# Kernel optimization log

Measured on AMD Instinct MI355X. Metric: run time of the kernel, lower is better.

The kernel has to match this reference:

```python
import jax, jax.numpy as jnp
import numpy as np

B = 32768      # rows
L = 512        # sequence_length
H = 1024       # inter_layer_size
E = 128        # encoding_size
K = 8          # number of (shifting_type, transformer_ID) combinations / decoders


def setup_inputs() -> dict:
    key = jax.random.key(0)
    ks = jax.random.split(key, 8)
    feats = jax.random.normal(ks[0], (B, L), jnp.float32)
    ids = jax.random.randint(ks[1], (B,), 0, K).astype(jnp.float32)
    x = jnp.concatenate([feats, ids[:, None]], axis=1)  # [B, L+1], last col = combination ID

    def init_w(k, shape, fan_in):
        return jax.random.normal(k, shape, jnp.float32) / np.float32(np.sqrt(fan_in))

    # shared encoder: Linear(L->H), Linear(H->E)  (weights stored [in, out])
    We1 = init_w(ks[2], (L, H), L); be1 = jnp.zeros((H,), jnp.float32)
    We2 = init_w(ks[3], (H, E), H); be2 = jnp.zeros((E,), jnp.float32)
    # per-ID decoders stacked along expert dim K: Linear(E->H), Linear(H->L)
    Wd1 = init_w(ks[4], (K, E, H), E); bd1 = jnp.zeros((K, H), jnp.float32)
    Wd2 = init_w(ks[5], (K, H, L), H); bd2 = jnp.zeros((K, L), jnp.float32)
    return dict(x=x, We1=We1, be1=be1, We2=We2, be2=be2,
                Wd1=Wd1, bd1=bd1, Wd2=Wd2, bd2=bd2)


def reference(x, We1, be1, We2, be2, Wd1, bd1, Wd2, bd2):
    seq_len = We1.shape[0]
    n_experts = Wd1.shape[0]
    ids = x[:, seq_len].astype(jnp.int32)          # routing column
    # torch code emits rows grouped by unique ID (torch.unique returns sorted ids);
    # jnp.argsort is stable, so within-group original order is preserved.
    order = jnp.argsort(ids)
    xs = x[order, :seq_len]                        # [B, L] grouped features
    ids_s = ids[order]                             # [B]

    # shared encoder MLP (LeakyReLU slope 0.01, torch default)
    h = jax.nn.leaky_relu(xs @ We1 + be1)          # [B, H]
    z = jax.nn.leaky_relu(h @ We2 + be2)           # [B, E]

    # dense expert dispatch: run every decoder, select per-row expert via one-hot
    hd = jax.nn.leaky_relu(jnp.einsum('be,keh->kbh', z, Wd1) + bd1[:, None, :])  # [K, B, H]
    y_all = jnp.einsum('kbh,khl->kbl', hd, Wd2) + bd2[:, None, :]                # [K, B, L]
    onehot = (ids_s[None, :] == jnp.arange(n_experts)[:, None]).astype(y_all.dtype)  # [K, B]
    return jnp.einsum('kb,kbl->bl', onehot, y_all)  # [B, L]
```

## Files before the change

### kernel.cpp

```cpp
#include <hip/hip_runtime.h>
#include <hip/hip_bf16.h>

#define B_ROWS 32768
#define L_DIM 512
#define H_DIM 1024
#define E_DIM 128
#define K_EXP 8
#define NBLK 128

typedef __bf16 bf16x8 __attribute__((ext_vector_type(8)));
typedef float f32x4 __attribute__((ext_vector_type(4)));

__device__ __forceinline__ void gload16(const void* src, void* dst) {
    __builtin_amdgcn_global_load_lds(
        (const __attribute__((address_space(1))) unsigned int*)src,
        (__attribute__((address_space(3))) unsigned int*)dst, 16, 0, 0);
}

__global__ void k_ids_hist(const float* __restrict__ x, int* __restrict__ ids,
                           int* __restrict__ hist) {
    __shared__ int lh[K_EXP];
    int t = threadIdx.x;
    if (t < K_EXP) lh[t] = 0;
    __syncthreads();
    int i = blockIdx.x * 256 + t;
    int id = (int)x[(size_t)i * (L_DIM + 1) + L_DIM];
    ids[i] = id;
    atomicAdd(&lh[id], 1);
    __syncthreads();
    if (t < K_EXP) hist[blockIdx.x * K_EXP + t] = lh[t];
}

__global__ void k_scan(const int* __restrict__ hist, int* __restrict__ base,
                       int* __restrict__ seg, int* __restrict__ tp) {
    __shared__ int c[K_EXP];
    __shared__ int sseg[K_EXP + 1];
    int k = threadIdx.x;
    if (k < K_EXP) {
        int run = 0;
        for (int b = 0; b < NBLK; ++b) {
            base[b * K_EXP + k] = run;
            run += hist[b * K_EXP + k];
        }
        c[k] = run;
    }
    __syncthreads();
    if (k == 0) {
        int s = 0, t2 = 0;
        for (int e = 0; e < K_EXP; ++e) {
            sseg[e] = s; seg[e] = s; tp[e] = t2;
            s += c[e]; t2 += (c[e] + 127) >> 7;
        }
        sseg[K_EXP] = s; seg[K_EXP] = s; tp[K_EXP] = t2;
    }
    __syncthreads();
    if (k < K_EXP) {
        int s0 = sseg[k];
        for (int b = 0; b < NBLK; ++b) base[b * K_EXP + k] += s0;
    }
}

__global__ void k_order(const int* __restrict__ ids, const int* __restrict__ base,
                        int* __restrict__ order) {
    __shared__ int sid[256];
    int t = threadIdx.x;
    int i = blockIdx.x * 256 + t;
    int my = ids[i];
    sid[t] = my;
    __syncthreads();
    int rank = 0;
    for (int j = 0; j < t; ++j) rank += (sid[j] == my) ? 1 : 0;
    order[base[blockIdx.x * K_EXP + my] + rank] = i;
}

__global__ void k_gather(const float* __restrict__ x, const int* __restrict__ order,
                         __hip_bfloat16* __restrict__ xs) {
    int idx = blockIdx.x * 256 + threadIdx.x;
    int p = idx >> 7;
    int c4 = (idx & 127) << 2;
    int src = order[p];
    const float* sp = x + (size_t)src * (L_DIM + 1) + c4;
    __hip_bfloat16 v[4];
    v[0] = __float2bfloat16(sp[0]);
    v[1] = __float2bfloat16(sp[1]);
    v[2] = __float2bfloat16(sp[2]);
    v[3] = __float2bfloat16(sp[3]);
    *(uint2*)(xs + (size_t)p * L_DIM + c4) = *(uint2*)v;
}

__global__ void k_transpose(const float* __restrict__ W, __hip_bfloat16* __restrict__ Wt,
                            int KDim, int NDim) {
    __shared__ float tile[32][33];
    int k0 = blockIdx.x << 5, n0 = blockIdx.y << 5;
    const float* Wb = W + (size_t)blockIdx.z * KDim * NDim;
    __hip_bfloat16* Wtb = Wt + (size_t)blockIdx.z * KDim * NDim;
    int tx = threadIdx.x & 31, ty = threadIdx.x >> 5;
    for (int i = ty; i < 32; i += 8)
        tile[i][tx] = Wb[(size_t)(k0 + i) * NDim + n0 + tx];
    __syncthreads();
    for (int i = ty; i < 32; i += 8)
        Wtb[(size_t)(n0 + i) * KDim + k0 + tx] = __float2bfloat16(tile[tx][i]);
}

template <int KD, int ND, bool GROUPED, bool LEAKY, bool OUT_BF16>
__launch_bounds__(256)
__global__ void gemm_mfma(const __hip_bfloat16* __restrict__ A,
                          const __hip_bfloat16* __restrict__ Bt,
                          const float* __restrict__ bias,
                          void* __restrict__ Cout,
                          const int* __restrict__ seg, const int* __restrict__ tp) {
    __shared__ __align__(16) __hip_bfloat16 smem[2 * 2 * 128 * 32];
    const int t = threadIdx.x;
    const int w = t >> 6, l = t & 63;
    const int n0 = blockIdx.y << 7;
    int m0, mEnd;
    const __hip_bfloat16* Bp = Bt;
    const float* bp = bias;
    if (GROUPED) {
        int bx = blockIdx.x;
        if (bx >= tp[K_EXP]) return;
        int e = 0;
        while (bx >= tp[e + 1]) ++e;
        m0 = seg[e] + ((bx - tp[e]) << 7);
        mEnd = seg[e + 1];
        Bp += (size_t)e * KD * ND;
        bp += (size_t)e * ND;
    } else {
        m0 = blockIdx.x << 7;
        mEnd = m0 + 128;
    }
    const int wm = w >> 1, wn = w & 1;
    const int g = l >> 4, li = l & 15;

    f32x4 acc[4][4];
#pragma unroll
    for (int i = 0; i < 4; ++i)
#pragma unroll
        for (int j = 0; j < 4; ++j) acc[i][j] = (f32x4){0.f, 0.f, 0.f, 0.f};

    auto stage = [&](int buf, int kt) {
#pragma unroll
        for (int qi = 0; qi < 2; ++qi) {
            int q = 2 * w + qi;
            int r = q * 16 + (l >> 2);
            int s = l & 3;
            int ksg = s ^ ((r >> 1) & 3);
            int rowg = m0 + r;
            if (GROUPED) rowg = min(rowg, B_ROWS - 1);
            const __hip_bfloat16* src = A + (size_t)rowg * KD + kt * 32 + ksg * 8;
            gload16(src, &smem[(buf * 2 + 0) * 4096 + q * 512]);
        }
#pragma unroll
        for (int qi = 0; qi < 2; ++qi) {
            int q = 2 * w + qi;
            int rc = q * 16 + (l >> 2);
            int s = l & 3;
            int ksg = s ^ ((rc >> 1) & 3);
            const __hip_bfloat16* src = Bp + (size_t)(n0 + rc) * KD + kt * 32 + ksg * 8;
            gload16(src, &smem[(buf * 2 + 1) * 4096 + q * 512]);
        }
    };

    constexpr int NK = KD / 32;
    stage(0, 0);
    for (int kt = 0; kt < NK; ++kt) {
        int buf = kt & 1;
        __syncthreads();
        if (kt + 1 < NK) stage(buf ^ 1, kt + 1);
        bf16x8 af[4], bfr[4];
#pragma unroll
        for (int fm = 0; fm < 4; ++fm) {
            int rr = wm * 64 + fm * 16 + li;
            int ss = g ^ ((rr >> 1) & 3);
            af[fm] = *(const bf16x8*)&smem[(buf * 2 + 0) * 4096 + rr * 32 + ss * 8];
        }
#pragma unroll
        for (int fn = 0; fn < 4; ++fn) {
            int cc = wn * 64 + fn * 16 + li;
            int ss = g ^ ((cc >> 1) & 3);
            bfr[fn] = *(const bf16x8*)&smem[(buf * 2 + 1) * 4096 + cc * 32 + ss * 8];
        }
#pragma unroll
        for (int fm = 0; fm < 4; ++fm)
#pragma unroll
            for (int fn = 0; fn < 4; ++fn)
                acc[fm][fn] = __builtin_amdgcn_mfma_f32_16x16x32_bf16(
                    af[fm], bfr[fn], acc[fm][fn], 0, 0, 0);
    }

    float bv[4];
#pragma unroll
    for (int fn = 0; fn < 4; ++fn) bv[fn] = bp[n0 + wn * 64 + fn * 16 + li];
#pragma unroll
    for (int fm = 0; fm < 4; ++fm) {
#pragma unroll
        for (int i = 0; i < 4; ++i) {
            int r = m0 + wm * 64 + fm * 16 + g * 4 + i;
            if (!GROUPED || r < mEnd) {
#pragma unroll
                for (int fn = 0; fn < 4; ++fn) {
                    float v = acc[fm][fn][i] + bv[fn];
                    if (LEAKY) v = v > 0.f ? v : 0.01f * v;
                    size_t off = (size_t)r * ND + n0 + wn * 64 + fn * 16 + li;
                    if (OUT_BF16)
                        ((__hip_bfloat16*)Cout)[off] = __float2bfloat16(v);
                    else
                        ((float*)Cout)[off] = v;
                }
            }
        }
    }
}

extern "C" void kernel_launch(void* const* d_in, const int* in_sizes, int n_in,
                              void* d_out, int out_size, void* d_ws, size_t ws_size,
                              hipStream_t stream) {
    (void)in_sizes; (void)n_in; (void)out_size; (void)ws_size;
    const float* x   = (const float*)d_in[0];
    const float* We1 = (const float*)d_in[1];
    const float* be1 = (const float*)d_in[2];
    const float* We2 = (const float*)d_in[3];
    const float* be2 = (const float*)d_in[4];
    const float* Wd1 = (const float*)d_in[5];
    const float* bd1 = (const float*)d_in[6];
    const float* Wd2 = (const float*)d_in[7];
    const float* bd2 = (const float*)d_in[8];
    float* out = (float*)d_out;

    char* w = (char*)d_ws;
    auto alloc = [&](size_t bytes) {
        char* p = w;
        w += (bytes + 255) & ~(size_t)255;
        return p;
    };
    int* ids   = (int*)alloc((size_t)B_ROWS * 4);
    int* order = (int*)alloc((size_t)B_ROWS * 4);
    int* hist  = (int*)alloc((size_t)NBLK * K_EXP * 4);
    int* base  = (int*)alloc((size_t)NBLK * K_EXP * 4);
    int* seg   = (int*)alloc((K_EXP + 1) * 4);
    int* tp    = (int*)alloc((K_EXP + 1) * 4);
    __hip_bfloat16* xs   = (__hip_bfloat16*)alloc((size_t)B_ROWS * L_DIM * 2);
    __hip_bfloat16* hbuf = (__hip_bfloat16*)alloc((size_t)B_ROWS * H_DIM * 2);
    __hip_bfloat16* zbuf = (__hip_bfloat16*)alloc((size_t)B_ROWS * E_DIM * 2);
    __hip_bfloat16* Wt1  = (__hip_bfloat16*)alloc((size_t)L_DIM * H_DIM * 2);
    __hip_bfloat16* Wt2  = (__hip_bfloat16*)alloc((size_t)H_DIM * E_DIM * 2);
    __hip_bfloat16* Wd1t = (__hip_bfloat16*)alloc((size_t)K_EXP * E_DIM * H_DIM * 2);
    __hip_bfloat16* Wd2t = (__hip_bfloat16*)alloc((size_t)K_EXP * H_DIM * L_DIM * 2);

    k_ids_hist<<<NBLK, 256, 0, stream>>>(x, ids, hist);
    k_scan<<<1, 64, 0, stream>>>(hist, base, seg, tp);
    k_order<<<NBLK, 256, 0, stream>>>(ids, base, order);
    k_gather<<<(B_ROWS * (L_DIM / 4)) / 256, 256, 0, stream>>>(x, order, xs);

    k_transpose<<<dim3(L_DIM / 32, H_DIM / 32, 1), 256, 0, stream>>>(We1, Wt1, L_DIM, H_DIM);
    k_transpose<<<dim3(H_DIM / 32, E_DIM / 32, 1), 256, 0, stream>>>(We2, Wt2, H_DIM, E_DIM);
    k_transpose<<<dim3(E_DIM / 32, H_DIM / 32, K_EXP), 256, 0, stream>>>(Wd1, Wd1t, E_DIM, H_DIM);
    k_transpose<<<dim3(H_DIM / 32, L_DIM / 32, K_EXP), 256, 0, stream>>>(Wd2, Wd2t, H_DIM, L_DIM);

    gemm_mfma<L_DIM, H_DIM, false, true, true>
        <<<dim3(B_ROWS / 128, H_DIM / 128), 256, 0, stream>>>(xs, Wt1, be1, hbuf, nullptr, nullptr);
    gemm_mfma<H_DIM, E_DIM, false, true, true>
        <<<dim3(B_ROWS / 128, E_DIM / 128), 256, 0, stream>>>(hbuf, Wt2, be2, zbuf, nullptr, nullptr);
    gemm_mfma<E_DIM, H_DIM, true, true, true>
        <<<dim3(B_ROWS / 128 + K_EXP, H_DIM / 128), 256, 0, stream>>>(zbuf, Wd1t, bd1, hbuf, seg, tp);
    gemm_mfma<H_DIM, L_DIM, true, false, false>
        <<<dim3(B_ROWS / 128 + K_EXP, L_DIM / 128), 256, 0, stream>>>(hbuf, Wd2t, bd2, out, seg, tp);
}
```

Baseline: 224.8 us.

## Fuse encoder GEMMs with LDS-resident hidden tile and pad expert segments

Fuses the two encoder GEMMs into one kernel. Each 128-row block computes 128-column chunks of the hidden layer, keeps them in LDS as bf16 and feeds them straight into the second GEMM, so the hidden activation never goes to global memory. Expert segments are padded to 128-row multiples with a per-tile expert map, which removes the per-block expert search and row clamping. Decoder output rows are remapped to compact positions at store time, and decoder blocks are swizzled across the grid. The trade-off is low occupancy in the fused kernel (one 256-thread block per CU, only up to 264 blocks) and Wt2 fragments read directly from global memory.

```diff
diff --git a/kernel.cpp b/kernel.cpp
--- a/kernel.cpp
+++ b/kernel.cpp
@@ -7,6 +7,8 @@
 #define E_DIM 128
 #define K_EXP 8
 #define NBLK 128
+#define MAXT 264
+#define MAXB (MAXT * 128)
 
 typedef __bf16 bf16x8 __attribute__((ext_vector_type(8)));
 typedef float f32x4 __attribute__((ext_vector_type(4)));
@@ -16,6 +18,12 @@
         (const __attribute__((address_space(1))) unsigned int*)src,
         (__attribute__((address_space(3))) unsigned int*)dst, 16, 0, 0);
 }
+
+#define M_NT 0
+#define M_SEG 1
+#define M_SEGP 10
+#define M_CNT 19
+#define M_TEXP 27
 
 __global__ void k_ids_hist(const float* __restrict__ x, int* __restrict__ ids,
                            int* __restrict__ hist) {
@@ -32,9 +40,10 @@
 }
 
 __global__ void k_scan(const int* __restrict__ hist, int* __restrict__ base,
-                       int* __restrict__ seg, int* __restrict__ tp) {
+                       int* __restrict__ meta, int* __restrict__ order_pad) {
     __shared__ int c[K_EXP];
-    __shared__ int sseg[K_EXP + 1];
+    __shared__ int sp[K_EXP + 1];
+    __shared__ int scnt[K_EXP];
     int k = threadIdx.x;
     if (k < K_EXP) {
         int run = 0;
@@ -46,18 +55,36 @@
     }
     __syncthreads();
     if (k == 0) {
-        int s = 0, t2 = 0;
+        int s = 0, p = 0;
         for (int e = 0; e < K_EXP; ++e) {
-            sseg[e] = s; seg[e] = s; tp[e] = t2;
-            s += c[e]; t2 += (c[e] + 127) >> 7;
-        }
-        sseg[K_EXP] = s; seg[K_EXP] = s; tp[K_EXP] = t2;
+            meta[M_SEG + e] = s;
+            meta[M_SEGP + e] = p;
+            meta[M_CNT + e] = c[e];
+            sp[e] = p;
+            scnt[e] = c[e];
+            s += c[e];
+            p += ((c[e] + 127) >> 7) << 7;
+        }
+        meta[M_SEG + K_EXP] = s;
+        meta[M_SEGP + K_EXP] = p;
+        sp[K_EXP] = p;
+        int nT = p >> 7;
+        meta[M_NT] = nT;
+        for (int e = 0; e < K_EXP; ++e)
+            for (int t2 = sp[e] >> 7; t2 < sp[e + 1] >> 7; ++t2)
+                meta[M_TEXP + t2] = e;
+        for (int t2 = nT; t2 < MAXT; ++t2) meta[M_TEXP + t2] = 0;
     }
     __syncthreads();
     if (k < K_EXP) {
-        int s0 = sseg[k];
+        int s0 = sp[k];
         for (int b = 0; b < NBLK; ++b) base[b * K_EXP + k] += s0;
     }
+    for (int e = 0; e < K_EXP; ++e) {
+        int st = sp[e] + scnt[e], en = sp[e + 1];
+        for (int p2 = st + k; p2 < en; p2 += 64) order_pad[p2] = 0;
+    }
+    for (int p2 = sp[K_EXP] + k; p2 < MAXB; p2 += 64) order_pad[p2] = 0;
 }
 
 __global__ void k_order(const int* __restrict__ ids, const int* __restrict__ base,
@@ -102,35 +129,167 @@
         Wtb[(size_t)(n0 + i) * KDim + k0 + tx] = __float2bfloat16(tile[tx][i]);
 }
 
-template <int KD, int ND, bool GROUPED, bool LEAKY, bool OUT_BF16>
+__launch_bounds__(256, 1)
+__global__ void k_enc(const __hip_bfloat16* __restrict__ xs,
+                      const __hip_bfloat16* __restrict__ Wt1,
+                      const __hip_bfloat16* __restrict__ Wt2,
+                      const float* __restrict__ be1,
+                      const float* __restrict__ be2,
+                      __hip_bfloat16* __restrict__ zb,
+                      const int* __restrict__ meta) {
+    __shared__ __align__(16) __hip_bfloat16 smem[2 * 2 * 128 * 32];
+    __shared__ __align__(16) __hip_bfloat16 hlds[4 * 128 * 32];
+    const int mt = blockIdx.x;
+    if (mt >= meta[M_NT]) return;
+    const int m0 = mt << 7;
+    const int t = threadIdx.x, w = t >> 6, l = t & 63;
+    const int wm = w >> 1, wn = w & 1, g = l >> 4, li = l & 15;
+    const int q0 = 2 * w, r0 = l >> 2, s0 = l & 3;
+
+    auto stageA = [&](int buf, int kt) {
+#pragma unroll
+        for (int qi = 0; qi < 2; ++qi) {
+            int q = q0 + qi, r = q * 16 + r0;
+            int ksg = s0 ^ ((r >> 1) & 3);
+            gload16(xs + (size_t)(m0 + r) * L_DIM + kt * 32 + ksg * 8,
+                    &smem[(buf * 2 + 0) * 4096 + q * 512]);
+        }
+    };
+    auto stageB = [&](int buf, int kt, int c) {
+#pragma unroll
+        for (int qi = 0; qi < 2; ++qi) {
+            int q = q0 + qi, r = q * 16 + r0;
+            int ksg = s0 ^ ((r >> 1) & 3);
+            gload16(Wt1 + (size_t)(c * 128 + r) * L_DIM + kt * 32 + ksg * 8,
+                    &smem[(buf * 2 + 1) * 4096 + q * 512]);
+        }
+    };
+
+    f32x4 accz[4][4];
+#pragma unroll
+    for (int i = 0; i < 4; ++i)
+#pragma unroll
+        for (int j = 0; j < 4; ++j) accz[i][j] = (f32x4){0.f, 0.f, 0.f, 0.f};
+
+    stageA(0, 0);
+    stageB(0, 0, 0);
+    for (int c = 0; c < 8; ++c) {
+        f32x4 acch[4][4];
+#pragma unroll
+        for (int i = 0; i < 4; ++i)
+#pragma unroll
+            for (int j = 0; j < 4; ++j) acch[i][j] = (f32x4){0.f, 0.f, 0.f, 0.f};
+
+        for (int kt = 0; kt < 16; ++kt) {
+            int buf = kt & 1;
+            __syncthreads();
+            if (kt < 15) { stageA(buf ^ 1, kt + 1); stageB(buf ^ 1, kt + 1, c); }
+            bf16x8 af[4], bfr[4];
+#pragma unroll
+            for (int fm = 0; fm < 4; ++fm) {
+                int rr = wm * 64 + fm * 16 + li;
+                int ss = g ^ ((rr >> 1) & 3);
+                af[fm] = *(const bf16x8*)&smem[(buf * 2 + 0) * 4096 + rr * 32 + ss * 8];
+            }
+#pragma unroll
+            for (int fn = 0; fn < 4; ++fn) {
+                int cc = wn * 64 + fn * 16 + li;
+                int ss = g ^ ((cc >> 1) & 3);
+                bfr[fn] = *(const bf16x8*)&smem[(buf * 2 + 1) * 4096 + cc * 32 + ss * 8];
+            }
+#pragma unroll
+            for (int fm = 0; fm < 4; ++fm)
+#pragma unroll
+                for (int fn = 0; fn < 4; ++fn)
+                    acch[fm][fn] = __builtin_amdgcn_mfma_f32_16x16x32_bf16(
+                        af[fm], bfr[fn], acch[fm][fn], 0, 0, 0);
+        }
+        __syncthreads();
+        if (c < 7) { stageA(0, 0); stageB(0, 0, c + 1); }
+
+        float bv1[4];
+#pragma unroll
+        for (int fn = 0; fn < 4; ++fn) bv1[fn] = be1[c * 128 + wn * 64 + fn * 16 + li];
+#pragma unroll
+        for (int fm = 0; fm < 4; ++fm)
+#pragma unroll
+            for (int i = 0; i < 4; ++i) {
+                int r = wm * 64 + fm * 16 + g * 4 + i;
+                int swr = (r >> 1) & 3;
+#pragma unroll
+                for (int fn = 0; fn < 4; ++fn) {
+                    int cc = wn * 64 + fn * 16 + li;
+                    float v = acch[fm][fn][i] + bv1[fn];
+                    v = v > 0.f ? v : 0.01f * v;
+                    int kblk = cc >> 5, k32 = cc & 31;
+                    hlds[kblk * 4096 + r * 32 + ((k32 >> 3) ^ swr) * 8 + (k32 & 7)] =
+                        __float2bfloat16(v);
+                }
+            }
+        __syncthreads();
+
+#pragma unroll
+        for (int kk = 0; kk < 4; ++kk) {
+            bf16x8 af2[4], bf2[4];
+#pragma unroll
+            for (int fm = 0; fm < 4; ++fm) {
+                int rr = wm * 64 + fm * 16 + li;
+                int ss = g ^ ((rr >> 1) & 3);
+                af2[fm] = *(const bf16x8*)&hlds[kk * 4096 + rr * 32 + ss * 8];
+            }
+#pragma unroll
+            for (int fn = 0; fn < 4; ++fn) {
+                int n = wn * 64 + fn * 16 + li;
+                bf2[fn] = *(const bf16x8*)(Wt2 + (size_t)n * H_DIM + c * 128 + kk * 32 + g * 8);
+            }
+#pragma unroll
+            for (int fm = 0; fm < 4; ++fm)
+#pragma unroll
+                for (int fn = 0; fn < 4; ++fn)
+                    accz[fm][fn] = __builtin_amdgcn_mfma_f32_16x16x32_bf16(
+                        af2[fm], bf2[fn], accz[fm][fn], 0, 0, 0);
+        }
+    }
+
+    float bv2[4];
+#pragma unroll
+    for (int fn = 0; fn < 4; ++fn) bv2[fn] = be2[wn * 64 + fn * 16 + li];
+#pragma unroll
+    for (int fm = 0; fm < 4; ++fm)
+#pragma unroll
+        for (int i = 0; i < 4; ++i) {
+            int r = m0 + wm * 64 + fm * 16 + g * 4 + i;
+#pragma unroll
+            for (int fn = 0; fn < 4; ++fn) {
+                float v = accz[fm][fn][i] + bv2[fn];
+                v = v > 0.f ? v : 0.01f * v;
+                zb[(size_t)r * E_DIM + wn * 64 + fn * 16 + li] = __float2bfloat16(v);
+            }
+        }
+}
+
+template <int KD, int ND, bool LEAKY, bool MAPROW>
 __launch_bounds__(256)
-__global__ void gemm_mfma(const __hip_bfloat16* __restrict__ A,
-                          const __hip_bfloat16* __restrict__ Bt,
-                          const float* __restrict__ bias,
-                          void* __restrict__ Cout,
-                          const int* __restrict__ seg, const int* __restrict__ tp) {
+__global__ void gemm_dec(const __hip_bfloat16* __restrict__ A,
+                         const __hip_bfloat16* __restrict__ Bt,
+                         const float* __restrict__ bias,
+                         void* __restrict__ Cout,
+                         const int* __restrict__ meta) {
     __shared__ __align__(16) __hip_bfloat16 smem[2 * 2 * 128 * 32];
-    const int t = threadIdx.x;
-    const int w = t >> 6, l = t & 63;
-    const int n0 = blockIdx.y << 7;
-    int m0, mEnd;
-    const __hip_bfloat16* Bp = Bt;
-    const float* bp = bias;
-    if (GROUPED) {
-        int bx = blockIdx.x;
-        if (bx >= tp[K_EXP]) return;
-        int e = 0;
-        while (bx >= tp[e + 1]) ++e;
-        m0 = seg[e] + ((bx - tp[e]) << 7);
-        mEnd = seg[e + 1];
-        Bp += (size_t)e * KD * ND;
-        bp += (size_t)e * ND;
-    } else {
-        m0 = blockIdx.x << 7;
-        mEnd = m0 + 128;
-    }
-    const int wm = w >> 1, wn = w & 1;
-    const int g = l >> 4, li = l & 15;
+    constexpr int NTN = ND / 128;
+    constexpr int TOT = NTN * MAXT;
+    int id = blockIdx.x;
+    int wg = (id & 7) * (TOT / 8) + (id >> 3);
+    int mt = wg / NTN, nt = wg % NTN;
+    if (mt >= meta[M_NT]) return;
+    const int e = meta[M_TEXP + mt];
+    const int m0 = mt << 7, n0 = nt << 7;
+    const __hip_bfloat16* Bp = Bt + (size_t)e * KD * ND;
+    const float* bp = bias + (size_t)e * ND;
+
+    const int t = threadIdx.x, w = t >> 6, l = t & 63;
+    const int wm = w >> 1, wn = w & 1, g = l >> 4, li = l & 15;
+    const int q0 = 2 * w, r0 = l >> 2, s0 = l & 3;
 
     f32x4 acc[4][4];
 #pragma unroll
@@ -141,23 +300,17 @@
     auto stage = [&](int buf, int kt) {
 #pragma unroll
         for (int qi = 0; qi < 2; ++qi) {
-            int q = 2 * w + qi;
-            int r = q * 16 + (l >> 2);
-            int s = l & 3;
-            int ksg = s ^ ((r >> 1) & 3);
-            int rowg = m0 + r;
-            if (GROUPED) rowg = min(rowg, B_ROWS - 1);
-            const __hip_bfloat16* src = A + (size_t)rowg * KD + kt * 32 + ksg * 8;
-            gload16(src, &smem[(buf * 2 + 0) * 4096 + q * 512]);
+            int q = q0 + qi, r = q * 16 + r0;
+            int ksg = s0 ^ ((r >> 1) & 3);
+            gload16(A + (size_t)(m0 + r) * KD + kt * 32 + ksg * 8,
+                    &smem[(buf * 2 + 0) * 4096 + q * 512]);
         }
 #pragma unroll
         for (int qi = 0; qi < 2; ++qi) {
-            int q = 2 * w + qi;
-            int rc = q * 16 + (l >> 2);
-            int s = l & 3;
-            int ksg = s ^ ((rc >> 1) & 3);
-            const __hip_bfloat16* src = Bp + (size_t)(n0 + rc) * KD + kt * 32 + ksg * 8;
-            gload16(src, &smem[(buf * 2 + 1) * 4096 + q * 512]);
+            int q = q0 + qi, r = q * 16 + r0;
+            int ksg = s0 ^ ((r >> 1) & 3);
+            gload16(Bp + (size_t)(n0 + r) * KD + kt * 32 + ksg * 8,
+                    &smem[(buf * 2 + 1) * 4096 + q * 512]);
         }
     };
 
@@ -191,25 +344,27 @@
     float bv[4];
 #pragma unroll
     for (int fn = 0; fn < 4; ++fn) bv[fn] = bp[n0 + wn * 64 + fn * 16 + li];
-#pragma unroll
-    for (int fm = 0; fm < 4; ++fm) {
+    int se = 0, sp2 = 0, ce = 0;
+    if (MAPROW) { se = meta[M_SEG + e]; sp2 = meta[M_SEGP + e]; ce = meta[M_CNT + e]; }
+#pragma unroll
+    for (int fm = 0; fm < 4; ++fm)
 #pragma unroll
         for (int i = 0; i < 4; ++i) {
-            int r = m0 + wm * 64 + fm * 16 + g * 4 + i;
-            if (!GROUPED || r < mEnd) {
-#pragma unroll
-                for (int fn = 0; fn < 4; ++fn) {
-                    float v = acc[fm][fn][i] + bv[fn];
-                    if (LEAKY) v = v > 0.f ? v : 0.01f * v;
-                    size_t off = (size_t)r * ND + n0 + wn * 64 + fn * 16 + li;
-                    if (OUT_BF16)
-                        ((__hip_bfloat16*)Cout)[off] = __float2bfloat16(v);
-                    else
-                        ((float*)Cout)[off] = v;
+            int rp = m0 + wm * 64 + fm * 16 + g * 4 + i;
+#pragma unroll
+            for (int fn = 0; fn < 4; ++fn) {
+                float v = acc[fm][fn][i] + bv[fn];
+                if (LEAKY) v = v > 0.f ? v : 0.01f * v;
+                int col = n0 + wn * 64 + fn * 16 + li;
+                if (MAPROW) {
+                    int local = rp - sp2;
+                    if (local < ce)
+                        ((float*)Cout)[(size_t)(se + local) * ND + col] = v;
+                } else {
+                    ((__hip_bfloat16*)Cout)[(size_t)rp * ND + col] = __float2bfloat16(v);
                 }
             }
         }
-    }
 }
 
 extern "C" void kernel_launch(void* const* d_in, const int* in_sizes, int n_in,
@@ -233,36 +388,32 @@
         w += (bytes + 255) & ~(size_t)255;
         return p;
     };
-    int* ids   = (int*)alloc((size_t)B_ROWS * 4);
-    int* order = (int*)alloc((size_t)B_ROWS * 4);
-    int* hist  = (int*)alloc((size_t)NBLK * K_EXP * 4);
-    int* base  = (int*)alloc((size_t)NBLK * K_EXP * 4);
-    int* seg   = (int*)alloc((K_EXP + 1) * 4);
-    int* tp    = (int*)alloc((K_EXP + 1) * 4);
-    __hip_bfloat16* xs   = (__hip_bfloat16*)alloc((size_t)B_ROWS * L_DIM * 2);
-    __hip_bfloat16* hbuf = (__hip_bfloat16*)alloc((size_t)B_ROWS * H_DIM * 2);
-    __hip_bfloat16* zbuf = (__hip_bfloat16*)alloc((size_t)B_ROWS * E_DIM * 2);
+    int* ids       = (int*)alloc((size_t)B_ROWS * 4);
+    int* order_pad = (int*)alloc((size_t)MAXB * 4);
+    int* hist      = (int*)alloc((size_t)NBLK * K_EXP * 4);
+    int* base      = (int*)alloc((size_t)NBLK * K_EXP * 4);
+    int* meta      = (int*)alloc((size_t)(M_TEXP + MAXT) * 4);
+    __hip_bfloat16* xs   = (__hip_bfloat16*)alloc((size_t)MAXB * L_DIM * 2);
+    __hip_bfloat16* zbuf = (__hip_bfloat16*)alloc((size_t)MAXB * E_DIM * 2);
+    __hip_bfloat16* hd   = (__hip_bfloat16*)alloc((size_t)MAXB * H_DIM * 2);
     __hip_bfloat16* Wt1  = (__hip_bfloat16*)alloc((size_t)L_DIM * H_DIM * 2);
     __hip_bfloat16* Wt2  = (__hip_bfloat16*)alloc((size_t)H_DIM * E_DIM * 2);
     __hip_bfloat16* Wd1t = (__hip_bfloat16*)alloc((size_t)K_EXP * E_DIM * H_DIM * 2);
     __hip_bfloat16* Wd2t = (__hip_bfloat16*)alloc((size_t)K_EXP * H_DIM * L_DIM * 2);
 
     k_ids_hist<<<NBLK, 256, 0, stream>>>(x, ids, hist);
-    k_scan<<<1, 64, 0, stream>>>(hist, base, seg, tp);
-    k_order<<<NBLK, 256, 0, stream>>>(ids, base, order);
-    k_gather<<<(B_ROWS * (L_DIM / 4)) / 256, 256, 0, stream>>>(x, order, xs);
+    k_scan<<<1, 64, 0, stream>>>(hist, base, meta, order_pad);
+    k_order<<<NBLK, 256, 0, stream>>>(ids, base, order_pad);
+    k_gather<<<(MAXB * (L_DIM / 4)) / 256, 256, 0, stream>>>(x, order_pad, xs);
 
     k_transpose<<<dim3(L_DIM / 32, H_DIM / 32, 1), 256, 0, stream>>>(We1, Wt1, L_DIM, H_DIM);
     k_transpose<<<dim3(H_DIM / 32, E_DIM / 32, 1), 256, 0, stream>>>(We2, Wt2, H_DIM, E_DIM);
     k_transpose<<<dim3(E_DIM / 32, H_DIM / 32, K_EXP), 256, 0, stream>>>(Wd1, Wd1t, E_DIM, H_DIM);
     k_transpose<<<dim3(H_DIM / 32, L_DIM / 32, K_EXP), 256, 0, stream>>>(Wd2, Wd2t, H_DIM, L_DIM);
 
-    gemm_mfma<L_DIM, H_DIM, false, true, true>
-        <<<dim3(B_ROWS / 128, H_DIM / 128), 256, 0, stream>>>(xs, Wt1, be1, hbuf, nullptr, nullptr);
-    gemm_mfma<H_DIM, E_DIM, false, true, true>
-        <<<dim3(B_ROWS / 128, E_DIM / 128), 256, 0, stream>>>(hbuf, Wt2, be2, zbuf, nullptr, nullptr);
-    gemm_mfma<E_DIM, H_DIM, true, true, true>
-        <<<dim3(B_ROWS / 128 + K_EXP, H_DIM / 128), 256, 0, stream>>>(zbuf, Wd1t, bd1, hbuf, seg, tp);
-    gemm_mfma<H_DIM, L_DIM, true, false, false>
-        <<<dim3(B_ROWS / 128 + K_EXP, L_DIM / 128), 256, 0, stream>>>(hbuf, Wd2t, bd2, out, seg, tp);
-}
+    k_enc<<<MAXT, 256, 0, stream>>>(xs, Wt1, Wt2, be1, be2, zbuf, meta);
+    gemm_dec<E_DIM, H_DIM, true, false>
+        <<<(H_DIM / 128) * MAXT, 256, 0, stream>>>(zbuf, Wd1t, bd1, hd, meta);
+    gemm_dec<H_DIM, L_DIM, false, true>
+        <<<(L_DIM / 128) * MAXT, 256, 0, stream>>>(hd, Wd2t, bd2, out, meta);
+}
```

New measurement: 333.9 us. 1.49x slower.

## Add triple-buffered GEMM with partial vmcnt waits and MFMA priority boost

Applied to the files above, without the earlier changes.

Adds a gemm_r3 variant that keeps three LDS stages in flight, prefetching two k-tiles ahead. It replaces __syncthreads with an explicit s_waitcnt vmcnt(4) plus s_barrier, so only the oldest stage's loads must finish before compute. MFMA sections are wrapped in s_setprio to favour matrix issue. It is used for the encoder GEMMs and the second decoder GEMM, which should hide more global-load latency at the cost of 50% more shared memory per block, which may lower occupancy.

```diff
diff --git a/kernel.cpp b/kernel.cpp
--- a/kernel.cpp
+++ b/kernel.cpp
@@ -100,6 +100,119 @@
     __syncthreads();
     for (int i = ty; i < 32; i += 8)
         Wtb[(size_t)(n0 + i) * KDim + k0 + tx] = __float2bfloat16(tile[tx][i]);
+}
+
+template <int KD, int ND, bool GROUPED, bool LEAKY, bool OUT_BF16>
+__launch_bounds__(256)
+__global__ void gemm_r3(const __hip_bfloat16* __restrict__ A,
+                        const __hip_bfloat16* __restrict__ Bt,
+                        const float* __restrict__ bias,
+                        void* __restrict__ Cout,
+                        const int* __restrict__ seg, const int* __restrict__ tp) {
+    __shared__ __align__(16) __hip_bfloat16 smem[3 * 2 * 128 * 32];
+    const int t = threadIdx.x;
+    const int w = t >> 6, l = t & 63;
+    const int n0 = blockIdx.y << 7;
+    int m0, mEnd;
+    const __hip_bfloat16* Bp = Bt;
+    const float* bp = bias;
+    if (GROUPED) {
+        int bx = blockIdx.x;
+        if (bx >= tp[K_EXP]) return;
+        int e = 0;
+        while (bx >= tp[e + 1]) ++e;
+        m0 = seg[e] + ((bx - tp[e]) << 7);
+        mEnd = seg[e + 1];
+        Bp += (size_t)e * KD * ND;
+        bp += (size_t)e * ND;
+    } else {
+        m0 = blockIdx.x << 7;
+        mEnd = m0 + 128;
+    }
+    const int wm = w >> 1, wn = w & 1, g = l >> 4, li = l & 15;
+    const int q0 = 2 * w, r0 = l >> 2, s0 = l & 3;
+
+    f32x4 acc[4][4];
+#pragma unroll
+    for (int i = 0; i < 4; ++i)
+#pragma unroll
+        for (int j = 0; j < 4; ++j) acc[i][j] = (f32x4){0.f, 0.f, 0.f, 0.f};
+
+    auto stage = [&](int b, int kt) {
+#pragma unroll
+        for (int qi = 0; qi < 2; ++qi) {
+            int q = q0 + qi, r = q * 16 + r0;
+            int ksg = s0 ^ ((r >> 1) & 3);
+            int rowg = m0 + r;
+            if (GROUPED) rowg = min(rowg, B_ROWS - 1);
+            gload16(A + (size_t)rowg * KD + kt * 32 + ksg * 8,
+                    &smem[b * 8192 + q * 512]);
+        }
+#pragma unroll
+        for (int qi = 0; qi < 2; ++qi) {
+            int q = q0 + qi, r = q * 16 + r0;
+            int ksg = s0 ^ ((r >> 1) & 3);
+            gload16(Bp + (size_t)(n0 + r) * KD + kt * 32 + ksg * 8,
+                    &smem[b * 8192 + 4096 + q * 512]);
+        }
+    };
+
+    constexpr int NK = KD / 32;
+    stage(0, 0);
+    stage(1, 1);
+    int b = 0;
+    for (int kt = 0; kt < NK; ++kt) {
+        if (kt == NK - 1)
+            asm volatile("s_waitcnt vmcnt(0)\ns_barrier" ::: "memory");
+        else
+            asm volatile("s_waitcnt vmcnt(4)\ns_barrier" ::: "memory");
+        __builtin_amdgcn_sched_barrier(0);
+        if (kt + 2 < NK) stage((b + 2 >= 3) ? b - 1 : b + 2, kt + 2);
+        bf16x8 af[4], bfr[4];
+#pragma unroll
+        for (int fm = 0; fm < 4; ++fm) {
+            int rr = wm * 64 + fm * 16 + li;
+            int ss = g ^ ((rr >> 1) & 3);
+            af[fm] = *(const bf16x8*)&smem[b * 8192 + rr * 32 + ss * 8];
+        }
+#pragma unroll
+        for (int fn = 0; fn < 4; ++fn) {
+            int cc = wn * 64 + fn * 16 + li;
+            int ss = g ^ ((cc >> 1) & 3);
+            bfr[fn] = *(const bf16x8*)&smem[b * 8192 + 4096 + cc * 32 + ss * 8];
+        }
+        __builtin_amdgcn_s_setprio(1);
+#pragma unroll
+        for (int fm = 0; fm < 4; ++fm)
+#pragma unroll
+            for (int fn = 0; fn < 4; ++fn)
+                acc[fm][fn] = __builtin_amdgcn_mfma_f32_16x16x32_bf16(
+                    af[fm], bfr[fn], acc[fm][fn], 0, 0, 0);
+        __builtin_amdgcn_s_setprio(0);
+        b = (b + 1 >= 3) ? 0 : b + 1;
+    }
+
+    float bv[4];
+#pragma unroll
+    for (int fn = 0; fn < 4; ++fn) bv[fn] = bp[n0 + wn * 64 + fn * 16 + li];
+#pragma unroll
+    for (int fm = 0; fm < 4; ++fm)
+#pragma unroll
+        for (int i = 0; i < 4; ++i) {
+            int r = m0 + wm * 64 + fm * 16 + g * 4 + i;
+            if (!GROUPED || r < mEnd) {
+#pragma unroll
+                for (int fn = 0; fn < 4; ++fn) {
+                    float v = acc[fm][fn][i] + bv[fn];
+                    if (LEAKY) v = v > 0.f ? v : 0.01f * v;
+                    size_t off = (size_t)r * ND + n0 + wn * 64 + fn * 16 + li;
+                    if (OUT_BF16)
+                        ((__hip_bfloat16*)Cout)[off] = __float2bfloat16(v);
+                    else
+                        ((float*)Cout)[off] = v;
+                }
+            }
+        }
 }
 
 template <int KD, int ND, bool GROUPED, bool LEAKY, bool OUT_BF16>
@@ -129,8 +242,8 @@
         m0 = blockIdx.x << 7;
         mEnd = m0 + 128;
     }
-    const int wm = w >> 1, wn = w & 1;
-    const int g = l >> 4, li = l & 15;
+    const int wm = w >> 1, wn = w & 1, g = l >> 4, li = l & 15;
+    const int q0 = 2 * w, r0 = l >> 2, s0 = l & 3;
 
     f32x4 acc[4][4];
 #pragma unroll
@@ -141,23 +254,19 @@
     auto stage = [&](int buf, int kt) {
 #pragma unroll
         for (int qi = 0; qi < 2; ++qi) {
-            int q = 2 * w + qi;
-            int r = q * 16 + (l >> 2);
-            int s = l & 3;
-            int ksg = s ^ ((r >> 1) & 3);
+            int q = q0 + qi, r = q * 16 + r0;
+            int ksg = s0 ^ ((r >> 1) & 3);
             int rowg = m0 + r;
             if (GROUPED) rowg = min(rowg, B_ROWS - 1);
-            const __hip_bfloat16* src = A + (size_t)rowg * KD + kt * 32 + ksg * 8;
-            gload16(src, &smem[(buf * 2 + 0) * 4096 + q * 512]);
+            gload16(A + (size_t)rowg * KD + kt * 32 + ksg * 8,
+                    &smem[(buf * 2 + 0) * 4096 + q * 512]);
         }
 #pragma unroll
         for (int qi = 0; qi < 2; ++qi) {
-            int q = 2 * w + qi;
-            int rc = q * 16 + (l >> 2);
-            int s = l & 3;
-            int ksg = s ^ ((rc >> 1) & 3);
-            const __hip_bfloat16* src = Bp + (size_t)(n0 + rc) * KD + kt * 32 + ksg * 8;
-            gload16(src, &smem[(buf * 2 + 1) * 4096 + q * 512]);
+            int q = q0 + qi, r = q * 16 + r0;
+            int ksg = s0 ^ ((r >> 1) & 3);
+            gload16(Bp + (size_t)(n0 + r) * KD + kt * 32 + ksg * 8,
+                    &smem[(buf * 2 + 1) * 4096 + q * 512]);
         }
     };
 
@@ -192,7 +301,7 @@
 #pragma unroll
     for (int fn = 0; fn < 4; ++fn) bv[fn] = bp[n0 + wn * 64 + fn * 16 + li];
 #pragma unroll
-    for (int fm = 0; fm < 4; ++fm) {
+    for (int fm = 0; fm < 4; ++fm)
 #pragma unroll
         for (int i = 0; i < 4; ++i) {
             int r = m0 + wm * 64 + fm * 16 + g * 4 + i;
@@ -209,7 +318,6 @@
                 }
             }
         }
-    }
 }
 
 extern "C" void kernel_launch(void* const* d_in, const int* in_sizes, int n_in,
@@ -257,12 +365,12 @@
     k_transpose<<<dim3(E_DIM / 32, H_DIM / 32, K_EXP), 256, 0, stream>>>(Wd1, Wd1t, E_DIM, H_DIM);
     k_transpose<<<dim3(H_DIM / 32, L_DIM / 32, K_EXP), 256, 0, stream>>>(Wd2, Wd2t, H_DIM, L_DIM);
 
-    gemm_mfma<L_DIM, H_DIM, false, true, true>
+    gemm_r3<L_DIM, H_DIM, false, true, true>
         <<<dim3(B_ROWS / 128, H_DIM / 128), 256, 0, stream>>>(xs, Wt1, be1, hbuf, nullptr, nullptr);
-    gemm_mfma<H_DIM, E_DIM, false, true, true>
+    gemm_r3<H_DIM, E_DIM, false, true, true>
         <<<dim3(B_ROWS / 128, E_DIM / 128), 256, 0, stream>>>(hbuf, Wt2, be2, zbuf, nullptr, nullptr);
     gemm_mfma<E_DIM, H_DIM, true, true, true>
         <<<dim3(B_ROWS / 128 + K_EXP, H_DIM / 128), 256, 0, stream>>>(zbuf, Wd1t, bd1, hbuf, seg, tp);
-    gemm_mfma<H_DIM, L_DIM, true, false, false>
+    gemm_r3<H_DIM, L_DIM, true, false, false>
         <<<dim3(B_ROWS / 128 + K_EXP, L_DIM / 128), 256, 0, stream>>>(hbuf, Wd2t, bd2, out, seg, tp);
 }
```

New measurement: 222.4 us. No clear change (-1.1%).

## Triple-buffer GEMM pipeline with XCD-aware tile remap and smaller M tile for encoder-2

Applied to the files above, without the earlier changes.

Rewrites the MFMA GEMM to use three LDS stages with two tiles prefetched ahead, waiting on a partial vmcnt plus a raw barrier instead of a full __syncthreads. Tiles are launched on a 1D grid and remapped so consecutive tile indices land on the same XCD chunk, which should improve L2 reuse. MFMA sections run at raised wave priority. The H->E GEMM uses 64-row tiles to give more blocks for its single N tile. The cost is more LDS per block, which may lower occupancy, and the hand-written vmcnt counts must match the number of loads issued per stage.

```diff
diff --git a/kernel.cpp b/kernel.cpp
--- a/kernel.cpp
+++ b/kernel.cpp
@@ -102,100 +102,119 @@
         Wtb[(size_t)(n0 + i) * KDim + k0 + tx] = __float2bfloat16(tile[tx][i]);
 }
 
-template <int KD, int ND, bool GROUPED, bool LEAKY, bool OUT_BF16>
+template <int BM, int KD, int ND, bool GROUPED, bool LEAKY, bool OUT_BF16>
 __launch_bounds__(256)
-__global__ void gemm_mfma(const __hip_bfloat16* __restrict__ A,
-                          const __hip_bfloat16* __restrict__ Bt,
-                          const float* __restrict__ bias,
-                          void* __restrict__ Cout,
-                          const int* __restrict__ seg, const int* __restrict__ tp) {
-    __shared__ __align__(16) __hip_bfloat16 smem[2 * 2 * 128 * 32];
-    const int t = threadIdx.x;
-    const int w = t >> 6, l = t & 63;
-    const int n0 = blockIdx.y << 7;
+__global__ void gemm_u(const __hip_bfloat16* __restrict__ A,
+                       const __hip_bfloat16* __restrict__ Bt,
+                       const float* __restrict__ bias,
+                       void* __restrict__ Cout,
+                       const int* __restrict__ seg, const int* __restrict__ tp) {
+    static_assert(!GROUPED || BM == 128, "grouped tiles are 128 rows");
+    constexpr int NNT = ND / 128;
+    constexpr int NMT = GROUPED ? (B_ROWS / 128 + K_EXP) : (B_ROWS / BM);
+    constexpr int TOT = NMT * NNT;
+    static_assert(TOT % 8 == 0, "XCD chunking needs TOT % 8 == 0");
+    constexpr int ACH = BM * 32;
+    constexpr int SLOT = ACH + 128 * 32;
+    constexpr int NK = KD / 32;
+    constexpr int VG = (BM == 128) ? 4 : 3;
+
+    __shared__ __align__(16) __hip_bfloat16 smem[3 * SLOT];
+    const int id = blockIdx.x;
+    const int wg = (id & 7) * (TOT / 8) + (id >> 3);
+    const int mt = wg / NNT, nt = wg % NNT;
+    const int n0 = nt << 7;
     int m0, mEnd;
     const __hip_bfloat16* Bp = Bt;
     const float* bp = bias;
     if (GROUPED) {
-        int bx = blockIdx.x;
-        if (bx >= tp[K_EXP]) return;
+        if (mt >= tp[K_EXP]) return;
         int e = 0;
-        while (bx >= tp[e + 1]) ++e;
-        m0 = seg[e] + ((bx - tp[e]) << 7);
+        while (mt >= tp[e + 1]) ++e;
+        m0 = seg[e] + ((mt - tp[e]) << 7);
         mEnd = seg[e + 1];
         Bp += (size_t)e * KD * ND;
         bp += (size_t)e * ND;
     } else {
-        m0 = blockIdx.x << 7;
-        mEnd = m0 + 128;
-    }
-    const int wm = w >> 1, wn = w & 1;
-    const int g = l >> 4, li = l & 15;
-
-    f32x4 acc[4][4];
-#pragma unroll
-    for (int i = 0; i < 4; ++i)
+        m0 = mt * BM;
+        mEnd = m0 + BM;
+    }
+    const int t = threadIdx.x, w = t >> 6, l = t & 63;
+    constexpr int FM = BM / 32;
+    const int wm = w >> 1, wn = w & 1, g = l >> 4, li = l & 15;
+    const int r0 = l >> 2, s0 = l & 3;
+
+    f32x4 acc[FM][4];
+#pragma unroll
+    for (int i = 0; i < FM; ++i)
 #pragma unroll
         for (int j = 0; j < 4; ++j) acc[i][j] = (f32x4){0.f, 0.f, 0.f, 0.f};
 
-    auto stage = [&](int buf, int kt) {
+    auto stage = [&](int b, int kt) {
+#pragma unroll
+        for (int qi = 0; qi < BM / 64; ++qi) {
+            int q = (BM / 64) * w + qi;
+            int r = q * 16 + r0;
+            int ksg = s0 ^ ((r >> 1) & 3);
+            int rowg = m0 + r;
+            if (GROUPED) rowg = min(rowg, B_ROWS - 1);
+            gload16(A + (size_t)rowg * KD + kt * 32 + ksg * 8,
+                    &smem[b * SLOT + q * 512]);
+        }
 #pragma unroll
         for (int qi = 0; qi < 2; ++qi) {
             int q = 2 * w + qi;
-            int r = q * 16 + (l >> 2);
-            int s = l & 3;
-            int ksg = s ^ ((r >> 1) & 3);
-            int rowg = m0 + r;
-            if (GROUPED) rowg = min(rowg, B_ROWS - 1);
-            const __hip_bfloat16* src = A + (size_t)rowg * KD + kt * 32 + ksg * 8;
-            gload16(src, &smem[(buf * 2 + 0) * 4096 + q * 512]);
-        }
-#pragma unroll
-        for (int qi = 0; qi < 2; ++qi) {
-            int q = 2 * w + qi;
-            int rc = q * 16 + (l >> 2);
-            int s = l & 3;
-            int ksg = s ^ ((rc >> 1) & 3);
-            const __hip_bfloat16* src = Bp + (size_t)(n0 + rc) * KD + kt * 32 + ksg * 8;
-            gload16(src, &smem[(buf * 2 + 1) * 4096 + q * 512]);
+            int r = q * 16 + r0;
+            int ksg = s0 ^ ((r >> 1) & 3);
+            gload16(Bp + (size_t)(n0 + r) * KD + kt * 32 + ksg * 8,
+                    &smem[b * SLOT + ACH + q * 512]);
         }
     };
 
-    constexpr int NK = KD / 32;
     stage(0, 0);
+    stage(1, 1);
+    int b = 0;
     for (int kt = 0; kt < NK; ++kt) {
-        int buf = kt & 1;
-        __syncthreads();
-        if (kt + 1 < NK) stage(buf ^ 1, kt + 1);
-        bf16x8 af[4], bfr[4];
-#pragma unroll
-        for (int fm = 0; fm < 4; ++fm) {
-            int rr = wm * 64 + fm * 16 + li;
+        if (kt == NK - 1)
+            asm volatile("s_waitcnt vmcnt(0)\ns_barrier" ::: "memory");
+        else if constexpr (VG == 4)
+            asm volatile("s_waitcnt vmcnt(4)\ns_barrier" ::: "memory");
+        else
+            asm volatile("s_waitcnt vmcnt(3)\ns_barrier" ::: "memory");
+        __builtin_amdgcn_sched_barrier(0);
+        if (kt + 2 < NK) stage((b + 2 >= 3) ? b - 1 : b + 2, kt + 2);
+        bf16x8 af[FM], bfr[4];
+#pragma unroll
+        for (int fm = 0; fm < FM; ++fm) {
+            int rr = wm * (FM * 16) + fm * 16 + li;
             int ss = g ^ ((rr >> 1) & 3);
-            af[fm] = *(const bf16x8*)&smem[(buf * 2 + 0) * 4096 + rr * 32 + ss * 8];
+            af[fm] = *(const bf16x8*)&smem[b * SLOT + rr * 32 + ss * 8];
         }
 #pragma unroll
         for (int fn = 0; fn < 4; ++fn) {
             int cc = wn * 64 + fn * 16 + li;
             int ss = g ^ ((cc >> 1) & 3);
-            bfr[fn] = *(const bf16x8*)&smem[(buf * 2 + 1) * 4096 + cc * 32 + ss * 8];
-        }
-#pragma unroll
-        for (int fm = 0; fm < 4; ++fm)
+            bfr[fn] = *(const bf16x8*)&smem[b * SLOT + ACH + cc * 32 + ss * 8];
+        }
+        __builtin_amdgcn_s_setprio(1);
+#pragma unroll
+        for (int fm = 0; fm < FM; ++fm)
 #pragma unroll
             for (int fn = 0; fn < 4; ++fn)
                 acc[fm][fn] = __builtin_amdgcn_mfma_f32_16x16x32_bf16(
                     af[fm], bfr[fn], acc[fm][fn], 0, 0, 0);
+        __builtin_amdgcn_s_setprio(0);
+        b = (b + 1 >= 3) ? 0 : b + 1;
     }
 
     float bv[4];
 #pragma unroll
     for (int fn = 0; fn < 4; ++fn) bv[fn] = bp[n0 + wn * 64 + fn * 16 + li];
 #pragma unroll
-    for (int fm = 0; fm < 4; ++fm) {
+    for (int fm = 0; fm < FM; ++fm)
 #pragma unroll
         for (int i = 0; i < 4; ++i) {
-            int r = m0 + wm * 64 + fm * 16 + g * 4 + i;
+            int r = m0 + wm * (FM * 16) + fm * 16 + g * 4 + i;
             if (!GROUPED || r < mEnd) {
 #pragma unroll
                 for (int fn = 0; fn < 4; ++fn) {
@@ -209,7 +228,6 @@
                 }
             }
         }
-    }
 }
 
 extern "C" void kernel_launch(void* const* d_in, const int* in_sizes, int n_in,
@@ -257,12 +275,12 @@
     k_transpose<<<dim3(E_DIM / 32, H_DIM / 32, K_EXP), 256, 0, stream>>>(Wd1, Wd1t, E_DIM, H_DIM);
     k_transpose<<<dim3(H_DIM / 32, L_DIM / 32, K_EXP), 256, 0, stream>>>(Wd2, Wd2t, H_DIM, L_DIM);
 
-    gemm_mfma<L_DIM, H_DIM, false, true, true>
-        <<<dim3(B_ROWS / 128, H_DIM / 128), 256, 0, stream>>>(xs, Wt1, be1, hbuf, nullptr, nullptr);
-    gemm_mfma<H_DIM, E_DIM, false, true, true>
-        <<<dim3(B_ROWS / 128, E_DIM / 128), 256, 0, stream>>>(hbuf, Wt2, be2, zbuf, nullptr, nullptr);
-    gemm_mfma<E_DIM, H_DIM, true, true, true>
-        <<<dim3(B_ROWS / 128 + K_EXP, H_DIM / 128), 256, 0, stream>>>(zbuf, Wd1t, bd1, hbuf, seg, tp);
-    gemm_mfma<H_DIM, L_DIM, true, false, false>
-        <<<dim3(B_ROWS / 128 + K_EXP, L_DIM / 128), 256, 0, stream>>>(hbuf, Wd2t, bd2, out, seg, tp);
-}
+    gemm_u<128, L_DIM, H_DIM, false, true, true>
+        <<<(B_ROWS / 128) * (H_DIM / 128), 256, 0, stream>>>(xs, Wt1, be1, hbuf, nullptr, nullptr);
+    gemm_u<64, H_DIM, E_DIM, false, true, true>
+        <<<(B_ROWS / 64) * (E_DIM / 128), 256, 0, stream>>>(hbuf, Wt2, be2, zbuf, nullptr, nullptr);
+    gemm_u<128, E_DIM, H_DIM, true, true, true>
+        <<<(B_ROWS / 128 + K_EXP) * (H_DIM / 128), 256, 0, stream>>>(zbuf, Wd1t, bd1, hbuf, seg, tp);
+    gemm_u<128, H_DIM, L_DIM, true, false, false>
+        <<<(B_ROWS / 128 + K_EXP) * (L_DIM / 128), 256, 0, stream>>>(hbuf, Wd2t, bd2, out, seg, tp);
+}
```

New measurement: 208.6 us. 1.08x faster.
